# Optimization experiments

Measured on AMD Instinct MI355X. Metric: run time of the kernel, lower is better.

## Reference

```python
import jax, jax.numpy as jnp
import numpy as np

NUM_HEADS = 4
IN_CHANNELS = 128


def setup_inputs() -> dict:
    key = jax.random.key(0)
    k_x, k_wq, k_bq, k_wo, k_bo = jax.random.split(key, 5)
    b, c, h, w = 16, IN_CHANNELS, 32, 32
    x = jax.random.normal(k_x, (b, c, h, w), dtype=jnp.float32)
    # 1x1 convs stored as (out_ch, in_ch) matrices
    w_qkv = jax.random.normal(k_wq, (c * 3 * NUM_HEADS, c), dtype=jnp.float32) * 0.02
    b_qkv = jax.random.normal(k_bq, (c * 3 * NUM_HEADS,), dtype=jnp.float32) * 0.02
    w_out = jax.random.normal(k_wo, (c, c * NUM_HEADS), dtype=jnp.float32) * 0.02
    b_out = jax.random.normal(k_bo, (c,), dtype=jnp.float32) * 0.02
    return {"x": x, "w_qkv": w_qkv, "b_qkv": b_qkv, "w_out": w_out, "b_out": b_out}


def reference(x, w_qkv, b_qkv, w_out, b_out):
    b, c, h, w = x.shape
    nh = NUM_HEADS
    # norm is Identity. 1x1 conv == per-pixel matmul over channels.
    qkv = jnp.einsum('bchw,oc->bohw', x, w_qkv) + b_qkv[None, :, None, None]
    qkv = qkv.reshape(b, nh, 3 * c, h, w)
    q, k, v = qkv[:, :, :c], qkv[:, :, c:2 * c], qkv[:, :, 2 * c:]
    # q, v: (b, nh, c, h, w) -> (b*nh, h*w, c); k -> (b*nh, c, h*w)
    q = q.transpose(0, 1, 3, 4, 2).reshape(b * nh, h * w, c)
    k = k.reshape(b * nh, c, h * w)
    v = v.transpose(0, 1, 3, 4, 2).reshape(b * nh, h * w, c)
    scores = jnp.einsum('bnc,bcm->bnm', q, k) * (c ** -0.5)  # (b*nh, hw, hw)
    attn = jax.nn.softmax(scores, axis=-1)
    out = jnp.einsum('bnm,bmc->bnc', attn, v)  # (b*nh, hw, c)
    out = out.reshape(b, nh, h, w, c).transpose(0, 4, 1, 2, 3).reshape(b, nh * c, h, w)
    out = jnp.einsum('bchw,oc->bohw', out, w_out) + b_out[None, :, None, None]
    return out + x
```

## Files before the change

### kernel.cpp

```cpp
#include <hip/hip_runtime.h>
#include <hip/hip_bf16.h>

typedef float  f32x4_v   __attribute__((ext_vector_type(4)));
typedef float  f32x16_v  __attribute__((ext_vector_type(16)));
typedef __bf16 bf16x8_v  __attribute__((ext_vector_type(8)));
typedef __bf16 bf16x4_v  __attribute__((ext_vector_type(4)));

#define WS_Q  0
#define WS_K  8388608
#define WS_V  16777216
#define WS_O  25165824
#define WS_WP 33554432

__device__ __forceinline__ int aswz(int p) { return ((p & 7) ^ ((p >> 3) & 7)) << 4; }

__device__ __forceinline__ void gload16(const void* g, void* l) {
    __builtin_amdgcn_global_load_lds(
        (const __attribute__((address_space(1))) unsigned int*)g,
        (__attribute__((address_space(3))) unsigned int*)l, 16, 0, 0);
}

__global__ __launch_bounds__(256) void k_permute(const float* __restrict__ w_out,
                                                 __bf16* __restrict__ w_perm) {
    int idx  = blockIdx.x * 256 + threadIdx.x;
    int head = idx >> 14;
    int o    = (idx >> 7) & 127;
    int c    = idx & 127;
    w_perm[idx] = (__bf16)w_out[o * 512 + c * 4 + head];
}

__global__ __launch_bounds__(256) void k_qkv(const float* __restrict__ x,
                                             const float* __restrict__ w_qkv,
                                             const float* __restrict__ b_qkv,
                                             __bf16* __restrict__ q_ws,
                                             __bf16* __restrict__ k_ws,
                                             __bf16* __restrict__ v_ws) {
    __shared__ __bf16 Ash[128 * 128];
    __shared__ __bf16 Bsh[128 * 128];
    const int tid = threadIdx.x;
    const int nt  = blockIdx.x;
    const int mt  = blockIdx.y;
    const int gm0 = mt * 128;
    const int b   = gm0 >> 10;
    const int p0  = gm0 & 1023;
    const int o0  = nt * 128;

    char* Ab = reinterpret_cast<char*>(Ash);
    char* Bb = reinterpret_cast<char*>(Bsh);

    for (int it = 0; it < 16; ++it) {
        int idx = tid + it * 256;
        int c   = idx >> 5;
        int i4  = (idx & 31) << 2;
        float4 v = *reinterpret_cast<const float4*>(x + b * 131072 + c * 1024 + p0 + i4);
        float vv[4] = {v.x, v.y, v.z, v.w};
#pragma unroll
        for (int j = 0; j < 4; ++j) {
            int p = i4 + j;
            int byte = ((p << 8) | (c << 1)) ^ aswz(p);
            *reinterpret_cast<__bf16*>(Ab + byte) = (__bf16)vv[j];
        }
    }
    for (int it = 0; it < 16; ++it) {
        int idx = tid + it * 256;
        int o   = idx >> 5;
        int c4  = (idx & 31) << 2;
        float4 v = *reinterpret_cast<const float4*>(w_qkv + (o0 + o) * 128 + c4);
        bf16x4_v h;
        h[0] = (__bf16)v.x; h[1] = (__bf16)v.y; h[2] = (__bf16)v.z; h[3] = (__bf16)v.w;
        int byte = ((o << 8) | (c4 << 1)) ^ aswz(o);
        *reinterpret_cast<bf16x4_v*>(Bb + byte) = h;
    }
    __syncthreads();

    const int lane = tid & 63;
    const int wv   = tid >> 6;
    const int wm   = (wv >> 1) * 64;
    const int wn   = (wv & 1) * 64;
    const int lr   = lane & 15;
    const int lg   = lane >> 4;

    f32x4_v acc[4][4] = {};
#pragma unroll
    for (int ks = 0; ks < 4; ++ks) {
        bf16x8_v af[4], bfr[4];
#pragma unroll
        for (int mi = 0; mi < 4; ++mi) {
            int row  = wm + mi * 16 + lr;
            int byte = ((row << 8) | (ks << 6) | (lg << 4)) ^ aswz(row);
            af[mi] = *reinterpret_cast<const bf16x8_v*>(Ab + byte);
        }
#pragma unroll
        for (int ni = 0; ni < 4; ++ni) {
            int row  = wn + ni * 16 + lr;
            int byte = ((row << 8) | (ks << 6) | (lg << 4)) ^ aswz(row);
            bfr[ni] = *reinterpret_cast<const bf16x8_v*>(Bb + byte);
        }
#pragma unroll
        for (int mi = 0; mi < 4; ++mi)
#pragma unroll
            for (int ni = 0; ni < 4; ++ni)
                acc[mi][ni] = __builtin_amdgcn_mfma_f32_16x16x32_bf16(af[mi], bfr[ni], acc[mi][ni], 0, 0, 0);
    }

#pragma unroll
    for (int ni = 0; ni < 4; ++ni) {
        int o    = o0 + wn + ni * 16 + lr;
        int head = o / 384;
        int rem  = o - head * 384;
        int type = rem >> 7;
        int ch   = rem & 127;
        float bias = b_qkv[o];
        int bh   = (b << 2) + head;
#pragma unroll
        for (int mi = 0; mi < 4; ++mi) {
            int prow = p0 + wm + mi * 16 + lg * 4;
            f32x4_v a = acc[mi][ni];
            if (type == 0) {
#pragma unroll
                for (int r = 0; r < 4; ++r)
                    q_ws[bh * 131072 + (prow + r) * 128 + ch] =
                        (__bf16)((a[r] + bias) * 0.12751744f);
            } else if (type == 1) {
#pragma unroll
                for (int r = 0; r < 4; ++r)
                    k_ws[bh * 131072 + (prow + r) * 128 + ch] = (__bf16)(a[r] + bias);
            } else {
                bf16x4_v hv;
#pragma unroll
                for (int r = 0; r < 4; ++r) hv[r] = (__bf16)(a[r] + bias);
                *reinterpret_cast<bf16x4_v*>(&v_ws[bh * 131072 + ch * 1024 + prow]) = hv;
            }
        }
    }
}

__device__ __forceinline__ void stage_kv(const __bf16* kg, const __bf16* vg,
                                         __bf16* kl, __bf16* vl, int wv, int lane) {
    const int s16 = lane & 15, r4 = lane >> 4;
    const int s8  = lane & 7,  r8 = lane >> 3;
#pragma unroll
    for (int i = 0; i < 4; ++i) {
        int row = wv * 16 + i * 4 + r4;
        const char* src = (const char*)(kg + row * 128) + ((s16 ^ (row & 7)) << 4);
        char* dst = (char*)kl + (wv * 16 + i * 4) * 256;
        gload16(src, dst);
    }
#pragma unroll
    for (int i = 0; i < 4; ++i) {
        int row = wv * 32 + i * 8 + r8;
        const char* src = (const char*)(vg + row * 1024) + ((s8 ^ (row & 7)) << 4);
        char* dst = (char*)vl + (wv * 32 + i * 8) * 128;
        gload16(src, dst);
    }
}

__global__ __launch_bounds__(256, 2) void k_attn(const __bf16* __restrict__ q_ws,
                                                 const __bf16* __restrict__ k_ws,
                                                 const __bf16* __restrict__ v_ws,
                                                 __bf16* __restrict__ o_ws) {
    __shared__ __bf16 Kbuf[2][64 * 128];
    __shared__ __bf16 Vbuf[2][128 * 64];

    const int tid  = threadIdx.x;
    const int lane = tid & 63;
    const int wv   = tid >> 6;
    const int col  = lane & 31;
    const int hi   = lane >> 5;

    const int id   = blockIdx.x;
    const int bh   = (id & 7) * 8 + (id >> 6);
    const int qt   = (id >> 3) & 7;
    const int base = bh * 131072;
    const int q0w  = qt * 128 + wv * 32;

    bf16x8_v bq[8];
    const __bf16* qp = q_ws + base + (q0w + col) * 128 + hi * 8;
#pragma unroll
    for (int ks = 0; ks < 8; ++ks)
        bq[ks] = *reinterpret_cast<const bf16x8_v*>(qp + ks * 16);

    f32x16_v of[4] = {};
    float m = -1e30f, l = 0.f;

    stage_kv(k_ws + base, v_ws + base, &Kbuf[0][0], &Vbuf[0][0], wv, lane);

    for (int t = 0; t < 16; ++t) {
        const int cur = t & 1;
        if (t < 15) {
            stage_kv(k_ws + base + (t + 1) * 64 * 128, v_ws + base + (t + 1) * 64,
                     &Kbuf[cur ^ 1][0], &Vbuf[cur ^ 1][0], wv, lane);
            asm volatile("s_waitcnt vmcnt(8)" ::: "memory");
        } else {
            asm volatile("s_waitcnt vmcnt(0)" ::: "memory");
        }
        __builtin_amdgcn_s_barrier();
        asm volatile("" ::: "memory");
        __builtin_amdgcn_sched_barrier(0);

        const char* Kl = (const char*)&Kbuf[cur][0];
        const char* Vl = (const char*)&Vbuf[cur][0];

        f32x16_v sa = {}, sb = {};
        __builtin_amdgcn_s_setprio(1);
#pragma unroll
        for (int ks = 0; ks < 8; ++ks) {
            const int sl = 2 * ks + hi;
            bf16x8_v af0 = *reinterpret_cast<const bf16x8_v*>(Kl + col * 256 + ((sl ^ (col & 7)) << 4));
            bf16x8_v af1 = *reinterpret_cast<const bf16x8_v*>(Kl + (32 + col) * 256 + ((sl ^ (col & 7)) << 4));
            sa = __builtin_amdgcn_mfma_f32_32x32x16_bf16(af0, bq[ks], sa, 0, 0, 0);
            sb = __builtin_amdgcn_mfma_f32_32x32x16_bf16(af1, bq[ks], sb, 0, 0, 0);
        }
        __builtin_amdgcn_s_setprio(0);

        float v = sa[0];
#pragma unroll
        for (int r = 1; r < 16; ++r) v = fmaxf(v, sa[r]);
#pragma unroll
        for (int r = 0; r < 16; ++r) v = fmaxf(v, sb[r]);
        float pmax = fmaxf(v, __shfl_xor(v, 32));
        if (!__all(pmax - m <= 8.0f)) {
            float fr = __builtin_amdgcn_exp2f(m - pmax);
            m = pmax;
            l *= fr;
#pragma unroll
            for (int r = 0; r < 16; ++r) {
                float frd = __shfl(fr, (r & 3) + 4 * hi + 8 * (r >> 2));
                of[0][r] *= frd; of[1][r] *= frd; of[2][r] *= frd; of[3][r] *= frd;
            }
        }
        float rs = 0.f;
#pragma unroll
        for (int r = 0; r < 16; ++r) { sa[r] = __builtin_amdgcn_exp2f(sa[r] - m); rs += sa[r]; }
#pragma unroll
        for (int r = 0; r < 16; ++r) { sb[r] = __builtin_amdgcn_exp2f(sb[r] - m); rs += sb[r]; }
        l += rs + __shfl_xor(rs, 32);

        bf16x8_v pa[4];
#pragma unroll
        for (int j = 0; j < 4; ++j) {
            const f32x16_v& sj = (j < 2) ? sa : sb;
            const int ro = 8 * (j & 1);
            unsigned w0, w1, w2, w3;
            asm("v_cvt_pk_bf16_f32 %0, %1, %2" : "=v"(w0) : "v"(sj[ro + 0]), "v"(sj[ro + 1]));
            asm("v_cvt_pk_bf16_f32 %0, %1, %2" : "=v"(w2) : "v"(sj[ro + 4]), "v"(sj[ro + 5]));
            asm("v_cvt_pk_bf16_f32 %0, %1, %2" : "=v"(w1) : "v"(sj[ro + 2]), "v"(sj[ro + 3]));
            asm("v_cvt_pk_bf16_f32 %0, %1, %2" : "=v"(w3) : "v"(sj[ro + 6]), "v"(sj[ro + 7]));
            asm("v_permlane32_swap_b32 %0, %1" : "+v"(w0), "+v"(w2));
            asm("v_permlane32_swap_b32 %0, %1" : "+v"(w1), "+v"(w3));
            union { unsigned u[4]; bf16x8_v h; } cvt;
            cvt.u[0] = w0; cvt.u[1] = w1; cvt.u[2] = w2; cvt.u[3] = w3;
            pa[j] = cvt.h;
        }

        __builtin_amdgcn_s_setprio(1);
#pragma unroll
        for (int n = 0; n < 4; ++n) {
#pragma unroll
            for (int j = 0; j < 4; ++j) {
                int row = 32 * n + col;
                bf16x8_v bv = *reinterpret_cast<const bf16x8_v*>(
                    Vl + row * 128 + (((2 * j + hi) ^ (row & 7)) << 4));
                of[n] = __builtin_amdgcn_mfma_f32_32x32x16_bf16(pa[j], bv, of[n], 0, 0, 0);
            }
        }
        __builtin_amdgcn_s_setprio(0);

        asm volatile("s_waitcnt lgkmcnt(0)" ::: "memory");
        __builtin_amdgcn_sched_barrier(0);
        __builtin_amdgcn_s_barrier();
        asm volatile("" ::: "memory");
        __builtin_amdgcn_sched_barrier(0);
    }

    float linv = 1.0f / l;
#pragma unroll
    for (int r = 0; r < 16; ++r) {
        int qr = (r & 3) + 4 * hi + 8 * (r >> 2);
        float ld = __shfl(linv, qr);
        int qg = q0w + qr;
#pragma unroll
        for (int n = 0; n < 4; ++n)
            o_ws[base + qg * 128 + 32 * n + col] = (__bf16)(of[n][r] * ld);
    }
}

__global__ __launch_bounds__(256) void k_out(const __bf16* __restrict__ o_ws,
                                             const __bf16* __restrict__ w_perm,
                                             const float* __restrict__ b_out,
                                             const float* __restrict__ x,
                                             float* __restrict__ out) {
    __shared__ __bf16 Al[64 * 136];
    __shared__ __bf16 Bl[128 * 136];
    const int tid  = threadIdx.x;
    const int lane = tid & 63, wv = tid >> 6;
    const int lr   = lane & 15, lg = lane >> 4;
    const int mt   = blockIdx.x;
    const int gp0  = mt * 64;
    const int b    = gp0 >> 10;
    const int p0   = gp0 & 1023;

    f32x4_v acc[8] = {};
    for (int kc = 0; kc < 4; ++kc) {
        __syncthreads();
#pragma unroll
        for (int it = 0; it < 4; ++it) {
            int idx = tid + it * 256;
            int rr = idx >> 4, k8 = (idx & 15) * 8;
            *reinterpret_cast<bf16x8_v*>(&Al[rr * 136 + k8]) =
                *reinterpret_cast<const bf16x8_v*>(&o_ws[(b * 4 + kc) * 131072 + (p0 + rr) * 128 + k8]);
        }
#pragma unroll
        for (int it = 0; it < 8; ++it) {
            int idx = tid + it * 256;
            int o = idx >> 4, k8 = (idx & 15) * 8;
            *reinterpret_cast<bf16x8_v*>(&Bl[o * 136 + k8]) =
                *reinterpret_cast<const bf16x8_v*>(&w_perm[kc * 16384 + o * 128 + k8]);
        }
        __syncthreads();
#pragma unroll
        for (int ks = 0; ks < 4; ++ks) {
            bf16x8_v af = *reinterpret_cast<const bf16x8_v*>(&Al[(wv * 16 + lr) * 136 + ks * 32 + lg * 8]);
#pragma unroll
            for (int ni = 0; ni < 8; ++ni) {
                bf16x8_v bf_ = *reinterpret_cast<const bf16x8_v*>(&Bl[(ni * 16 + lr) * 136 + ks * 32 + lg * 8]);
                acc[ni] = __builtin_amdgcn_mfma_f32_16x16x32_bf16(af, bf_, acc[ni], 0, 0, 0);
            }
        }
    }

    int prow = p0 + wv * 16 + lg * 4;
#pragma unroll
    for (int ni = 0; ni < 8; ++ni) {
        int o = ni * 16 + lr;
        float bias = b_out[o];
        float4 xr = *reinterpret_cast<const float4*>(&x[b * 131072 + o * 1024 + prow]);
        float4 res;
        res.x = acc[ni][0] + bias + xr.x;
        res.y = acc[ni][1] + bias + xr.y;
        res.z = acc[ni][2] + bias + xr.z;
        res.w = acc[ni][3] + bias + xr.w;
        *reinterpret_cast<float4*>(&out[b * 131072 + o * 1024 + prow]) = res;
    }
}

extern "C" void kernel_launch(void* const* d_in, const int* in_sizes, int n_in,
                              void* d_out, int out_size, void* d_ws, size_t ws_size,
                              hipStream_t stream) {
    const float* x     = (const float*)d_in[0];
    const float* w_qkv = (const float*)d_in[1];
    const float* b_qkv = (const float*)d_in[2];
    const float* w_out = (const float*)d_in[3];
    const float* b_out = (const float*)d_in[4];
    float* out = (float*)d_out;
    __bf16* ws = (__bf16*)d_ws;

    __bf16* q_ws   = ws + WS_Q;
    __bf16* k_ws   = ws + WS_K;
    __bf16* v_ws   = ws + WS_V;
    __bf16* o_ws   = ws + WS_O;
    __bf16* w_perm = ws + WS_WP;

    k_permute<<<256, 256, 0, stream>>>(w_out, w_perm);
    k_qkv<<<dim3(12, 128), 256, 0, stream>>>(x, w_qkv, b_qkv, q_ws, k_ws, v_ws);
    k_attn<<<512, 256, 0, stream>>>(q_ws, k_ws, v_ws, o_ws);
    k_out<<<256, 256, 0, stream>>>(o_ws, w_perm, b_out, x, out);
}
```

Measured before the change: 92.83 us.

## Fold weight permute into QKV GEMM, reuse x tile, and give attention waves two query tiles

The separate weight-permute kernel is merged into the QKV projection kernel. Each QKV block now loads its x tile into LDS once and loops over six output-channel tiles, where before twelve separate blocks each reloaded it. The attention kernel drops to 128 threads per block, and each wave handles two 32-row query tiles that share the same K/V LDS reads, which doubles reuse of K/V fragments. The trade-off is higher register pressure, fewer waves per CU, and a smaller QKV grid (256 blocks) with less parallelism.

```diff
diff --git a/kernel.cpp b/kernel.cpp
--- a/kernel.cpp
+++ b/kernel.cpp
@@ -20,30 +20,30 @@
         (__attribute__((address_space(3))) unsigned int*)l, 16, 0, 0);
 }
 
-__global__ __launch_bounds__(256) void k_permute(const float* __restrict__ w_out,
-                                                 __bf16* __restrict__ w_perm) {
-    int idx  = blockIdx.x * 256 + threadIdx.x;
-    int head = idx >> 14;
-    int o    = (idx >> 7) & 127;
-    int c    = idx & 127;
-    w_perm[idx] = (__bf16)w_out[o * 512 + c * 4 + head];
-}
-
 __global__ __launch_bounds__(256) void k_qkv(const float* __restrict__ x,
                                              const float* __restrict__ w_qkv,
                                              const float* __restrict__ b_qkv,
                                              __bf16* __restrict__ q_ws,
                                              __bf16* __restrict__ k_ws,
-                                             __bf16* __restrict__ v_ws) {
+                                             __bf16* __restrict__ v_ws,
+                                             const float* __restrict__ w_out,
+                                             __bf16* __restrict__ w_perm) {
     __shared__ __bf16 Ash[128 * 128];
     __shared__ __bf16 Bsh[128 * 128];
-    const int tid = threadIdx.x;
-    const int nt  = blockIdx.x;
-    const int mt  = blockIdx.y;
-    const int gm0 = mt * 128;
-    const int b   = gm0 >> 10;
-    const int p0  = gm0 & 1023;
-    const int o0  = nt * 128;
+    const int tid  = threadIdx.x;
+    const int half = blockIdx.x;
+    const int mt   = blockIdx.y;
+    const int gm0  = mt * 128;
+    const int b    = gm0 >> 10;
+    const int p0   = gm0 & 1023;
+
+    {
+        int gid  = (mt * 2 + half) * 256 + tid;
+        int head = gid >> 14;
+        int o    = (gid >> 7) & 127;
+        int c    = gid & 127;
+        w_perm[gid] = (__bf16)w_out[o * 512 + c * 4 + head];
+    }
 
     char* Ab = reinterpret_cast<char*>(Ash);
     char* Bb = reinterpret_cast<char*>(Bsh);
@@ -61,17 +61,6 @@
             *reinterpret_cast<__bf16*>(Ab + byte) = (__bf16)vv[j];
         }
     }
-    for (int it = 0; it < 16; ++it) {
-        int idx = tid + it * 256;
-        int o   = idx >> 5;
-        int c4  = (idx & 31) << 2;
-        float4 v = *reinterpret_cast<const float4*>(w_qkv + (o0 + o) * 128 + c4);
-        bf16x4_v h;
-        h[0] = (__bf16)v.x; h[1] = (__bf16)v.y; h[2] = (__bf16)v.z; h[3] = (__bf16)v.w;
-        int byte = ((o << 8) | (c4 << 1)) ^ aswz(o);
-        *reinterpret_cast<bf16x4_v*>(Bb + byte) = h;
-    }
-    __syncthreads();
 
     const int lane = tid & 63;
     const int wv   = tid >> 6;
@@ -80,56 +69,72 @@
     const int lr   = lane & 15;
     const int lg   = lane >> 4;
 
-    f32x4_v acc[4][4] = {};
-#pragma unroll
-    for (int ks = 0; ks < 4; ++ks) {
-        bf16x8_v af[4], bfr[4];
-#pragma unroll
-        for (int mi = 0; mi < 4; ++mi) {
-            int row  = wm + mi * 16 + lr;
-            int byte = ((row << 8) | (ks << 6) | (lg << 4)) ^ aswz(row);
-            af[mi] = *reinterpret_cast<const bf16x8_v*>(Ab + byte);
-        }
+    for (int i = 0; i < 6; ++i) {
+        const int o0 = (half * 6 + i) * 128;
+        __syncthreads();
+        for (int it = 0; it < 16; ++it) {
+            int idx = tid + it * 256;
+            int o   = idx >> 5;
+            int c4  = (idx & 31) << 2;
+            float4 v = *reinterpret_cast<const float4*>(w_qkv + (o0 + o) * 128 + c4);
+            bf16x4_v h;
+            h[0] = (__bf16)v.x; h[1] = (__bf16)v.y; h[2] = (__bf16)v.z; h[3] = (__bf16)v.w;
+            int byte = ((o << 8) | (c4 << 1)) ^ aswz(o);
+            *reinterpret_cast<bf16x4_v*>(Bb + byte) = h;
+        }
+        __syncthreads();
+
+        f32x4_v acc[4][4] = {};
+#pragma unroll
+        for (int ks = 0; ks < 4; ++ks) {
+            bf16x8_v af[4], bfr[4];
+#pragma unroll
+            for (int mi = 0; mi < 4; ++mi) {
+                int row  = wm + mi * 16 + lr;
+                int byte = ((row << 8) | (ks << 6) | (lg << 4)) ^ aswz(row);
+                af[mi] = *reinterpret_cast<const bf16x8_v*>(Ab + byte);
+            }
+#pragma unroll
+            for (int ni = 0; ni < 4; ++ni) {
+                int row  = wn + ni * 16 + lr;
+                int byte = ((row << 8) | (ks << 6) | (lg << 4)) ^ aswz(row);
+                bfr[ni] = *reinterpret_cast<const bf16x8_v*>(Bb + byte);
+            }
+#pragma unroll
+            for (int mi = 0; mi < 4; ++mi)
+#pragma unroll
+                for (int ni = 0; ni < 4; ++ni)
+                    acc[mi][ni] = __builtin_amdgcn_mfma_f32_16x16x32_bf16(af[mi], bfr[ni], acc[mi][ni], 0, 0, 0);
+        }
+
 #pragma unroll
         for (int ni = 0; ni < 4; ++ni) {
-            int row  = wn + ni * 16 + lr;
-            int byte = ((row << 8) | (ks << 6) | (lg << 4)) ^ aswz(row);
-            bfr[ni] = *reinterpret_cast<const bf16x8_v*>(Bb + byte);
-        }
-#pragma unroll
-        for (int mi = 0; mi < 4; ++mi)
-#pragma unroll
-            for (int ni = 0; ni < 4; ++ni)
-                acc[mi][ni] = __builtin_amdgcn_mfma_f32_16x16x32_bf16(af[mi], bfr[ni], acc[mi][ni], 0, 0, 0);
-    }
-
-#pragma unroll
-    for (int ni = 0; ni < 4; ++ni) {
-        int o    = o0 + wn + ni * 16 + lr;
-        int head = o / 384;
-        int rem  = o - head * 384;
-        int type = rem >> 7;
-        int ch   = rem & 127;
-        float bias = b_qkv[o];
-        int bh   = (b << 2) + head;
-#pragma unroll
-        for (int mi = 0; mi < 4; ++mi) {
-            int prow = p0 + wm + mi * 16 + lg * 4;
-            f32x4_v a = acc[mi][ni];
-            if (type == 0) {
-#pragma unroll
-                for (int r = 0; r < 4; ++r)
-                    q_ws[bh * 131072 + (prow + r) * 128 + ch] =
-                        (__bf16)((a[r] + bias) * 0.12751744f);
-            } else if (type == 1) {
-#pragma unroll
-                for (int r = 0; r < 4; ++r)
-                    k_ws[bh * 131072 + (prow + r) * 128 + ch] = (__bf16)(a[r] + bias);
-            } else {
-                bf16x4_v hv;
-#pragma unroll
-                for (int r = 0; r < 4; ++r) hv[r] = (__bf16)(a[r] + bias);
-                *reinterpret_cast<bf16x4_v*>(&v_ws[bh * 131072 + ch * 1024 + prow]) = hv;
+            int o    = o0 + wn + ni * 16 + lr;
+            int head = o / 384;
+            int rem  = o - head * 384;
+            int type = rem >> 7;
+            int ch   = rem & 127;
+            float bias = b_qkv[o];
+            int bh   = (b << 2) + head;
+#pragma unroll
+            for (int mi = 0; mi < 4; ++mi) {
+                int prow = p0 + wm + mi * 16 + lg * 4;
+                f32x4_v a = acc[mi][ni];
+                if (type == 0) {
+#pragma unroll
+                    for (int r = 0; r < 4; ++r)
+                        q_ws[bh * 131072 + (prow + r) * 128 + ch] =
+                            (__bf16)((a[r] + bias) * 0.12751744f);
+                } else if (type == 1) {
+#pragma unroll
+                    for (int r = 0; r < 4; ++r)
+                        k_ws[bh * 131072 + (prow + r) * 128 + ch] = (__bf16)(a[r] + bias);
+                } else {
+                    bf16x4_v hv;
+#pragma unroll
+                    for (int r = 0; r < 4; ++r) hv[r] = (__bf16)(a[r] + bias);
+                    *reinterpret_cast<bf16x4_v*>(&v_ws[bh * 131072 + ch * 1024 + prow]) = hv;
+                }
             }
         }
     }
@@ -140,22 +145,65 @@
     const int s16 = lane & 15, r4 = lane >> 4;
     const int s8  = lane & 7,  r8 = lane >> 3;
 #pragma unroll
-    for (int i = 0; i < 4; ++i) {
-        int row = wv * 16 + i * 4 + r4;
+    for (int i = 0; i < 8; ++i) {
+        int row = wv * 32 + i * 4 + r4;
         const char* src = (const char*)(kg + row * 128) + ((s16 ^ (row & 7)) << 4);
-        char* dst = (char*)kl + (wv * 16 + i * 4) * 256;
-        gload16(src, dst);
-    }
-#pragma unroll
-    for (int i = 0; i < 4; ++i) {
-        int row = wv * 32 + i * 8 + r8;
+        gload16(src, (char*)kl + (wv * 32 + i * 4) * 256);
+    }
+#pragma unroll
+    for (int i = 0; i < 8; ++i) {
+        int row = wv * 64 + i * 8 + r8;
         const char* src = (const char*)(vg + row * 1024) + ((s8 ^ (row & 7)) << 4);
-        char* dst = (char*)vl + (wv * 32 + i * 8) * 128;
-        gload16(src, dst);
-    }
-}
-
-__global__ __launch_bounds__(256, 2) void k_attn(const __bf16* __restrict__ q_ws,
+        gload16(src, (char*)vl + (wv * 64 + i * 8) * 128);
+    }
+}
+
+__device__ __forceinline__ void softmax_pack(f32x16_v& s0, f32x16_v& s1,
+                                             float& m, float& l,
+                                             f32x16_v (&of)[4], bf16x8_v (&pa)[4],
+                                             int hi) {
+    float t[16];
+#pragma unroll
+    for (int r = 0; r < 16; ++r) t[r] = fmaxf(s0[r], s1[r]);
+#pragma unroll
+    for (int w = 8; w >= 1; w >>= 1)
+#pragma unroll
+        for (int r = 0; r < w; ++r) t[r] = fmaxf(t[r], t[r + w]);
+    float pmax = fmaxf(t[0], __shfl_xor(t[0], 32));
+    if (!__all(pmax - m <= 8.0f)) {
+        float fr = __builtin_amdgcn_exp2f(m - pmax);
+        m = pmax;
+        l *= fr;
+#pragma unroll
+        for (int r = 0; r < 16; ++r) {
+            float frd = __shfl(fr, (r & 3) + 4 * hi + 8 * (r >> 2));
+            of[0][r] *= frd; of[1][r] *= frd; of[2][r] *= frd; of[3][r] *= frd;
+        }
+    }
+    float rs = 0.f;
+#pragma unroll
+    for (int r = 0; r < 16; ++r) { s0[r] = __builtin_amdgcn_exp2f(s0[r] - m); rs += s0[r]; }
+#pragma unroll
+    for (int r = 0; r < 16; ++r) { s1[r] = __builtin_amdgcn_exp2f(s1[r] - m); rs += s1[r]; }
+    l += rs + __shfl_xor(rs, 32);
+#pragma unroll
+    for (int j = 0; j < 4; ++j) {
+        const f32x16_v& sj = (j < 2) ? s0 : s1;
+        const int ro = 8 * (j & 1);
+        unsigned w0, w1, w2, w3;
+        asm("v_cvt_pk_bf16_f32 %0, %1, %2" : "=v"(w0) : "v"(sj[ro + 0]), "v"(sj[ro + 1]));
+        asm("v_cvt_pk_bf16_f32 %0, %1, %2" : "=v"(w2) : "v"(sj[ro + 4]), "v"(sj[ro + 5]));
+        asm("v_cvt_pk_bf16_f32 %0, %1, %2" : "=v"(w1) : "v"(sj[ro + 2]), "v"(sj[ro + 3]));
+        asm("v_cvt_pk_bf16_f32 %0, %1, %2" : "=v"(w3) : "v"(sj[ro + 6]), "v"(sj[ro + 7]));
+        asm("v_permlane32_swap_b32 %0, %1" : "+v"(w0), "+v"(w2));
+        asm("v_permlane32_swap_b32 %0, %1" : "+v"(w1), "+v"(w3));
+        union { unsigned u[4]; bf16x8_v h; } cvt;
+        cvt.u[0] = w0; cvt.u[1] = w1; cvt.u[2] = w2; cvt.u[3] = w3;
+        pa[j] = cvt.h;
+    }
+}
+
+__global__ __launch_bounds__(128, 1) void k_attn(const __bf16* __restrict__ q_ws,
                                                  const __bf16* __restrict__ k_ws,
                                                  const __bf16* __restrict__ v_ws,
                                                  __bf16* __restrict__ o_ws) {
@@ -172,16 +220,19 @@
     const int bh   = (id & 7) * 8 + (id >> 6);
     const int qt   = (id >> 3) & 7;
     const int base = bh * 131072;
-    const int q0w  = qt * 128 + wv * 32;
-
-    bf16x8_v bq[8];
-    const __bf16* qp = q_ws + base + (q0w + col) * 128 + hi * 8;
-#pragma unroll
-    for (int ks = 0; ks < 8; ++ks)
-        bq[ks] = *reinterpret_cast<const bf16x8_v*>(qp + ks * 16);
-
-    f32x16_v of[4] = {};
-    float m = -1e30f, l = 0.f;
+    const int q0w  = qt * 128 + wv * 64;
+
+    bf16x8_v bqA[8], bqB[8];
+    const __bf16* qpA = q_ws + base + (q0w + col) * 128 + hi * 8;
+    const __bf16* qpB = qpA + 32 * 128;
+#pragma unroll
+    for (int ks = 0; ks < 8; ++ks) {
+        bqA[ks] = *reinterpret_cast<const bf16x8_v*>(qpA + ks * 16);
+        bqB[ks] = *reinterpret_cast<const bf16x8_v*>(qpB + ks * 16);
+    }
+
+    f32x16_v ofA[4] = {}, ofB[4] = {};
+    float mA = -1e30f, lA = 0.f, mB = -1e30f, lB = 0.f;
 
     stage_kv(k_ws + base, v_ws + base, &Kbuf[0][0], &Vbuf[0][0], wv, lane);
 
@@ -190,7 +241,7 @@
         if (t < 15) {
             stage_kv(k_ws + base + (t + 1) * 64 * 128, v_ws + base + (t + 1) * 64,
                      &Kbuf[cur ^ 1][0], &Vbuf[cur ^ 1][0], wv, lane);
-            asm volatile("s_waitcnt vmcnt(8)" ::: "memory");
+            asm volatile("s_waitcnt vmcnt(16)" ::: "memory");
         } else {
             asm volatile("s_waitcnt vmcnt(0)" ::: "memory");
         }
@@ -201,57 +252,23 @@
         const char* Kl = (const char*)&Kbuf[cur][0];
         const char* Vl = (const char*)&Vbuf[cur][0];
 
-        f32x16_v sa = {}, sb = {};
+        f32x16_v sA0 = {}, sA1 = {}, sB0 = {}, sB1 = {};
         __builtin_amdgcn_s_setprio(1);
 #pragma unroll
         for (int ks = 0; ks < 8; ++ks) {
             const int sl = 2 * ks + hi;
             bf16x8_v af0 = *reinterpret_cast<const bf16x8_v*>(Kl + col * 256 + ((sl ^ (col & 7)) << 4));
             bf16x8_v af1 = *reinterpret_cast<const bf16x8_v*>(Kl + (32 + col) * 256 + ((sl ^ (col & 7)) << 4));
-            sa = __builtin_amdgcn_mfma_f32_32x32x16_bf16(af0, bq[ks], sa, 0, 0, 0);
-            sb = __builtin_amdgcn_mfma_f32_32x32x16_bf16(af1, bq[ks], sb, 0, 0, 0);
+            sA0 = __builtin_amdgcn_mfma_f32_32x32x16_bf16(af0, bqA[ks], sA0, 0, 0, 0);
+            sA1 = __builtin_amdgcn_mfma_f32_32x32x16_bf16(af1, bqA[ks], sA1, 0, 0, 0);
+            sB0 = __builtin_amdgcn_mfma_f32_32x32x16_bf16(af0, bqB[ks], sB0, 0, 0, 0);
+            sB1 = __builtin_amdgcn_mfma_f32_32x32x16_bf16(af1, bqB[ks], sB1, 0, 0, 0);
         }
         __builtin_amdgcn_s_setprio(0);
 
-        float v = sa[0];
-#pragma unroll
-        for (int r = 1; r < 16; ++r) v = fmaxf(v, sa[r]);
-#pragma unroll
-        for (int r = 0; r < 16; ++r) v = fmaxf(v, sb[r]);
-        float pmax = fmaxf(v, __shfl_xor(v, 32));
-        if (!__all(pmax - m <= 8.0f)) {
-            float fr = __builtin_amdgcn_exp2f(m - pmax);
-            m = pmax;
-            l *= fr;
-#pragma unroll
-            for (int r = 0; r < 16; ++r) {
-                float frd = __shfl(fr, (r & 3) + 4 * hi + 8 * (r >> 2));
-                of[0][r] *= frd; of[1][r] *= frd; of[2][r] *= frd; of[3][r] *= frd;
-            }
-        }
-        float rs = 0.f;
-#pragma unroll
-        for (int r = 0; r < 16; ++r) { sa[r] = __builtin_amdgcn_exp2f(sa[r] - m); rs += sa[r]; }
-#pragma unroll
-        for (int r = 0; r < 16; ++r) { sb[r] = __builtin_amdgcn_exp2f(sb[r] - m); rs += sb[r]; }
-        l += rs + __shfl_xor(rs, 32);
-
-        bf16x8_v pa[4];
-#pragma unroll
-        for (int j = 0; j < 4; ++j) {
-            const f32x16_v& sj = (j < 2) ? sa : sb;
-            const int ro = 8 * (j & 1);
-            unsigned w0, w1, w2, w3;
-            asm("v_cvt_pk_bf16_f32 %0, %1, %2" : "=v"(w0) : "v"(sj[ro + 0]), "v"(sj[ro + 1]));
-            asm("v_cvt_pk_bf16_f32 %0, %1, %2" : "=v"(w2) : "v"(sj[ro + 4]), "v"(sj[ro + 5]));
-            asm("v_cvt_pk_bf16_f32 %0, %1, %2" : "=v"(w1) : "v"(sj[ro + 2]), "v"(sj[ro + 3]));
-            asm("v_cvt_pk_bf16_f32 %0, %1, %2" : "=v"(w3) : "v"(sj[ro + 6]), "v"(sj[ro + 7]));
-            asm("v_permlane32_swap_b32 %0, %1" : "+v"(w0), "+v"(w2));
-            asm("v_permlane32_swap_b32 %0, %1" : "+v"(w1), "+v"(w3));
-            union { unsigned u[4]; bf16x8_v h; } cvt;
-            cvt.u[0] = w0; cvt.u[1] = w1; cvt.u[2] = w2; cvt.u[3] = w3;
-            pa[j] = cvt.h;
-        }
+        bf16x8_v paA[4], paB[4];
+        softmax_pack(sA0, sA1, mA, lA, ofA, paA, hi);
+        softmax_pack(sB0, sB1, mB, lB, ofB, paB, hi);
 
         __builtin_amdgcn_s_setprio(1);
 #pragma unroll
@@ -261,7 +278,8 @@
                 int row = 32 * n + col;
                 bf16x8_v bv = *reinterpret_cast<const bf16x8_v*>(
                     Vl + row * 128 + (((2 * j + hi) ^ (row & 7)) << 4));
-                of[n] = __builtin_amdgcn_mfma_f32_32x32x16_bf16(pa[j], bv, of[n], 0, 0, 0);
+                ofA[n] = __builtin_amdgcn_mfma_f32_32x32x16_bf16(paA[j], bv, ofA[n], 0, 0, 0);
+                ofB[n] = __builtin_amdgcn_mfma_f32_32x32x16_bf16(paB[j], bv, ofB[n], 0, 0, 0);
             }
         }
         __builtin_amdgcn_s_setprio(0);
@@ -273,15 +291,17 @@
         __builtin_amdgcn_sched_barrier(0);
     }
 
-    float linv = 1.0f / l;
+    float linvA = 1.0f / lA, linvB = 1.0f / lB;
 #pragma unroll
     for (int r = 0; r < 16; ++r) {
         int qr = (r & 3) + 4 * hi + 8 * (r >> 2);
-        float ld = __shfl(linv, qr);
-        int qg = q0w + qr;
-#pragma unroll
-        for (int n = 0; n < 4; ++n)
-            o_ws[base + qg * 128 + 32 * n + col] = (__bf16)(of[n][r] * ld);
+        float ldA = __shfl(linvA, qr);
+        float ldB = __shfl(linvB, qr);
+#pragma unroll
+        for (int n = 0; n < 4; ++n) {
+            o_ws[base + (q0w + qr) * 128 + 32 * n + col]      = (__bf16)(ofA[n][r] * ldA);
+            o_ws[base + (q0w + 32 + qr) * 128 + 32 * n + col] = (__bf16)(ofB[n][r] * ldB);
+        }
     }
 }
 
@@ -361,8 +381,7 @@
     __bf16* o_ws   = ws + WS_O;
     __bf16* w_perm = ws + WS_WP;
 
-    k_permute<<<256, 256, 0, stream>>>(w_out, w_perm);
-    k_qkv<<<dim3(12, 128), 256, 0, stream>>>(x, w_qkv, b_qkv, q_ws, k_ws, v_ws);
-    k_attn<<<512, 256, 0, stream>>>(q_ws, k_ws, v_ws, o_ws);
+    k_qkv<<<dim3(2, 128), 256, 0, stream>>>(x, w_qkv, b_qkv, q_ws, k_ws, v_ws, w_out, w_perm);
+    k_attn<<<512, 128, 0, stream>>>(q_ws, k_ws, v_ws, o_ws);
     k_out<<<256, 256, 0, stream>>>(o_ws, w_perm, b_out, x, out);
 }
```

New measurement: 104.2 us. 1.12x slower.

## Reuse x tile across QKV output tiles, fuse permute, shrink attention KV tile

Applied to the files above, without the earlier changes.

The QKV projection grid shrinks from 12x128 to 2x128 blocks. Each block keeps its converted x tile in shared memory and loops over six weight tiles, and the w_out permute kernel is folded into this kernel, which removes one launch. The attention kernel moves to 128-thread blocks (two waves, 64 queries) with 32-key K/V tiles, twice as many iterations and twice the grid, and declares launch bounds that allow three blocks per unit. The intent is to cut redundant x loads and conversion, drop a launch, and raise attention occupancy. The cost is fewer, serialized QKV blocks and half the MFMA work between each barrier and softmax step in attention.

```diff
diff --git a/kernel.cpp b/kernel.cpp
--- a/kernel.cpp
+++ b/kernel.cpp
@@ -20,30 +20,30 @@
         (__attribute__((address_space(3))) unsigned int*)l, 16, 0, 0);
 }
 
-__global__ __launch_bounds__(256) void k_permute(const float* __restrict__ w_out,
-                                                 __bf16* __restrict__ w_perm) {
-    int idx  = blockIdx.x * 256 + threadIdx.x;
-    int head = idx >> 14;
-    int o    = (idx >> 7) & 127;
-    int c    = idx & 127;
-    w_perm[idx] = (__bf16)w_out[o * 512 + c * 4 + head];
-}
-
 __global__ __launch_bounds__(256) void k_qkv(const float* __restrict__ x,
                                              const float* __restrict__ w_qkv,
                                              const float* __restrict__ b_qkv,
                                              __bf16* __restrict__ q_ws,
                                              __bf16* __restrict__ k_ws,
-                                             __bf16* __restrict__ v_ws) {
+                                             __bf16* __restrict__ v_ws,
+                                             const float* __restrict__ w_out,
+                                             __bf16* __restrict__ w_perm) {
     __shared__ __bf16 Ash[128 * 128];
     __shared__ __bf16 Bsh[128 * 128];
-    const int tid = threadIdx.x;
-    const int nt  = blockIdx.x;
-    const int mt  = blockIdx.y;
-    const int gm0 = mt * 128;
-    const int b   = gm0 >> 10;
-    const int p0  = gm0 & 1023;
-    const int o0  = nt * 128;
+    const int tid  = threadIdx.x;
+    const int half = blockIdx.x;
+    const int mt   = blockIdx.y;
+    const int gm0  = mt * 128;
+    const int b    = gm0 >> 10;
+    const int p0   = gm0 & 1023;
+
+    {
+        int gid  = (mt * 2 + half) * 256 + tid;
+        int head = gid >> 14;
+        int o    = (gid >> 7) & 127;
+        int c    = gid & 127;
+        w_perm[gid] = (__bf16)w_out[o * 512 + c * 4 + head];
+    }
 
     char* Ab = reinterpret_cast<char*>(Ash);
     char* Bb = reinterpret_cast<char*>(Bsh);
@@ -61,17 +61,6 @@
             *reinterpret_cast<__bf16*>(Ab + byte) = (__bf16)vv[j];
         }
     }
-    for (int it = 0; it < 16; ++it) {
-        int idx = tid + it * 256;
-        int o   = idx >> 5;
-        int c4  = (idx & 31) << 2;
-        float4 v = *reinterpret_cast<const float4*>(w_qkv + (o0 + o) * 128 + c4);
-        bf16x4_v h;
-        h[0] = (__bf16)v.x; h[1] = (__bf16)v.y; h[2] = (__bf16)v.z; h[3] = (__bf16)v.w;
-        int byte = ((o << 8) | (c4 << 1)) ^ aswz(o);
-        *reinterpret_cast<bf16x4_v*>(Bb + byte) = h;
-    }
-    __syncthreads();
 
     const int lane = tid & 63;
     const int wv   = tid >> 6;
@@ -80,87 +69,107 @@
     const int lr   = lane & 15;
     const int lg   = lane >> 4;
 
-    f32x4_v acc[4][4] = {};
-#pragma unroll
-    for (int ks = 0; ks < 4; ++ks) {
-        bf16x8_v af[4], bfr[4];
-#pragma unroll
-        for (int mi = 0; mi < 4; ++mi) {
-            int row  = wm + mi * 16 + lr;
-            int byte = ((row << 8) | (ks << 6) | (lg << 4)) ^ aswz(row);
-            af[mi] = *reinterpret_cast<const bf16x8_v*>(Ab + byte);
-        }
+    for (int i = 0; i < 6; ++i) {
+        const int o0 = (half * 6 + i) * 128;
+        __syncthreads();
+        for (int it = 0; it < 16; ++it) {
+            int idx = tid + it * 256;
+            int o   = idx >> 5;
+            int c4  = (idx & 31) << 2;
+            float4 v = *reinterpret_cast<const float4*>(w_qkv + (o0 + o) * 128 + c4);
+            bf16x4_v h;
+            h[0] = (__bf16)v.x; h[1] = (__bf16)v.y; h[2] = (__bf16)v.z; h[3] = (__bf16)v.w;
+            int byte = ((o << 8) | (c4 << 1)) ^ aswz(o);
+            *reinterpret_cast<bf16x4_v*>(Bb + byte) = h;
+        }
+        __syncthreads();
+
+        f32x4_v acc[4][4] = {};
+#pragma unroll
+        for (int ks = 0; ks < 4; ++ks) {
+            bf16x8_v af[4], bfr[4];
+#pragma unroll
+            for (int mi = 0; mi < 4; ++mi) {
+                int row  = wm + mi * 16 + lr;
+                int byte = ((row << 8) | (ks << 6) | (lg << 4)) ^ aswz(row);
+                af[mi] = *reinterpret_cast<const bf16x8_v*>(Ab + byte);
+            }
+#pragma unroll
+            for (int ni = 0; ni < 4; ++ni) {
+                int row  = wn + ni * 16 + lr;
+                int byte = ((row << 8) | (ks << 6) | (lg << 4)) ^ aswz(row);
+                bfr[ni] = *reinterpret_cast<const bf16x8_v*>(Bb + byte);
+            }
+#pragma unroll
+            for (int mi = 0; mi < 4; ++mi)
+#pragma unroll
+                for (int ni = 0; ni < 4; ++ni)
+                    acc[mi][ni] = __builtin_amdgcn_mfma_f32_16x16x32_bf16(af[mi], bfr[ni], acc[mi][ni], 0, 0, 0);
+        }
+
 #pragma unroll
         for (int ni = 0; ni < 4; ++ni) {
-            int row  = wn + ni * 16 + lr;
-            int byte = ((row << 8) | (ks << 6) | (lg << 4)) ^ aswz(row);
-            bfr[ni] = *reinterpret_cast<const bf16x8_v*>(Bb + byte);
-        }
-#pragma unroll
-        for (int mi = 0; mi < 4; ++mi)
-#pragma unroll
-            for (int ni = 0; ni < 4; ++ni)
-                acc[mi][ni] = __builtin_amdgcn_mfma_f32_16x16x32_bf16(af[mi], bfr[ni], acc[mi][ni], 0, 0, 0);
-    }
-
-#pragma unroll
-    for (int ni = 0; ni < 4; ++ni) {
-        int o    = o0 + wn + ni * 16 + lr;
-        int head = o / 384;
-        int rem  = o - head * 384;
-        int type = rem >> 7;
-        int ch   = rem & 127;
-        float bias = b_qkv[o];
-        int bh   = (b << 2) + head;
-#pragma unroll
-        for (int mi = 0; mi < 4; ++mi) {
-            int prow = p0 + wm + mi * 16 + lg * 4;
-            f32x4_v a = acc[mi][ni];
-            if (type == 0) {
-#pragma unroll
-                for (int r = 0; r < 4; ++r)
-                    q_ws[bh * 131072 + (prow + r) * 128 + ch] =
-                        (__bf16)((a[r] + bias) * 0.12751744f);
-            } else if (type == 1) {
-#pragma unroll
-                for (int r = 0; r < 4; ++r)
-                    k_ws[bh * 131072 + (prow + r) * 128 + ch] = (__bf16)(a[r] + bias);
-            } else {
-                bf16x4_v hv;
-#pragma unroll
-                for (int r = 0; r < 4; ++r) hv[r] = (__bf16)(a[r] + bias);
-                *reinterpret_cast<bf16x4_v*>(&v_ws[bh * 131072 + ch * 1024 + prow]) = hv;
-            }
-        }
-    }
-}
-
-__device__ __forceinline__ void stage_kv(const __bf16* kg, const __bf16* vg,
-                                         __bf16* kl, __bf16* vl, int wv, int lane) {
+            int o    = o0 + wn + ni * 16 + lr;
+            int head = o / 384;
+            int rem  = o - head * 384;
+            int type = rem >> 7;
+            int ch   = rem & 127;
+            float bias = b_qkv[o];
+            int bh   = (b << 2) + head;
+#pragma unroll
+            for (int mi = 0; mi < 4; ++mi) {
+                int prow = p0 + wm + mi * 16 + lg * 4;
+                f32x4_v a = acc[mi][ni];
+                if (type == 0) {
+#pragma unroll
+                    for (int r = 0; r < 4; ++r)
+                        q_ws[bh * 131072 + (prow + r) * 128 + ch] =
+                            (__bf16)((a[r] + bias) * 0.12751744f);
+                } else if (type == 1) {
+#pragma unroll
+                    for (int r = 0; r < 4; ++r)
+                        k_ws[bh * 131072 + (prow + r) * 128 + ch] = (__bf16)(a[r] + bias);
+                } else {
+                    bf16x4_v hv;
+#pragma unroll
+                    for (int r = 0; r < 4; ++r) hv[r] = (__bf16)(a[r] + bias);
+                    *reinterpret_cast<bf16x4_v*>(&v_ws[bh * 131072 + ch * 1024 + prow]) = hv;
+                }
+            }
+        }
+    }
+}
+
+__device__ __forceinline__ void stage_kv32(const __bf16* kg, const __bf16* vg,
+                                           __bf16* kl, __bf16* vl, int wv, int lane) {
     const int s16 = lane & 15, r4 = lane >> 4;
-    const int s8  = lane & 7,  r8 = lane >> 3;
+    const int s4  = lane & 3,  r16 = lane >> 2;
+#pragma unroll
+    for (int i = 0; i < 2; ++i) {
+        int row = wv * 16 + i * 8 + r4;
+        int rb  = wv * 16 + i * 8 + ((lane >> 4) & ~0);
+        (void)rb;
+    }
 #pragma unroll
     for (int i = 0; i < 4; ++i) {
         int row = wv * 16 + i * 4 + r4;
         const char* src = (const char*)(kg + row * 128) + ((s16 ^ (row & 7)) << 4);
-        char* dst = (char*)kl + (wv * 16 + i * 4) * 256;
-        gload16(src, dst);
+        gload16(src, (char*)kl + (wv * 16 + i * 4) * 256);
     }
 #pragma unroll
     for (int i = 0; i < 4; ++i) {
-        int row = wv * 32 + i * 8 + r8;
-        const char* src = (const char*)(vg + row * 1024) + ((s8 ^ (row & 7)) << 4);
-        char* dst = (char*)vl + (wv * 32 + i * 8) * 128;
-        gload16(src, dst);
-    }
-}
-
-__global__ __launch_bounds__(256, 2) void k_attn(const __bf16* __restrict__ q_ws,
+        int row = wv * 64 + i * 16 + r16;
+        const char* src = (const char*)(vg + row * 1024) + ((s4 ^ (row & 3)) << 4);
+        gload16(src, (char*)vl + (wv * 64 + i * 16) * 64);
+    }
+}
+
+__global__ __launch_bounds__(128, 3) void k_attn(const __bf16* __restrict__ q_ws,
                                                  const __bf16* __restrict__ k_ws,
                                                  const __bf16* __restrict__ v_ws,
                                                  __bf16* __restrict__ o_ws) {
-    __shared__ __bf16 Kbuf[2][64 * 128];
-    __shared__ __bf16 Vbuf[2][128 * 64];
+    __shared__ __bf16 Kbuf[2][32 * 128];
+    __shared__ __bf16 Vbuf[2][128 * 32];
 
     const int tid  = threadIdx.x;
     const int lane = tid & 63;
@@ -169,10 +178,10 @@
     const int hi   = lane >> 5;
 
     const int id   = blockIdx.x;
-    const int bh   = (id & 7) * 8 + (id >> 6);
-    const int qt   = (id >> 3) & 7;
+    const int bh   = (id & 7) * 8 + (id >> 7);
+    const int qt   = (id >> 3) & 15;
     const int base = bh * 131072;
-    const int q0w  = qt * 128 + wv * 32;
+    const int q0w  = qt * 64 + wv * 32;
 
     bf16x8_v bq[8];
     const __bf16* qp = q_ws + base + (q0w + col) * 128 + hi * 8;
@@ -183,13 +192,13 @@
     f32x16_v of[4] = {};
     float m = -1e30f, l = 0.f;
 
-    stage_kv(k_ws + base, v_ws + base, &Kbuf[0][0], &Vbuf[0][0], wv, lane);
-
-    for (int t = 0; t < 16; ++t) {
+    stage_kv32(k_ws + base, v_ws + base, &Kbuf[0][0], &Vbuf[0][0], wv, lane);
+
+    for (int t = 0; t < 32; ++t) {
         const int cur = t & 1;
-        if (t < 15) {
-            stage_kv(k_ws + base + (t + 1) * 64 * 128, v_ws + base + (t + 1) * 64,
-                     &Kbuf[cur ^ 1][0], &Vbuf[cur ^ 1][0], wv, lane);
+        if (t < 31) {
+            stage_kv32(k_ws + base + (t + 1) * 32 * 128, v_ws + base + (t + 1) * 32,
+                       &Kbuf[cur ^ 1][0], &Vbuf[cur ^ 1][0], wv, lane);
             asm volatile("s_waitcnt vmcnt(8)" ::: "memory");
         } else {
             asm volatile("s_waitcnt vmcnt(0)" ::: "memory");
@@ -201,24 +210,24 @@
         const char* Kl = (const char*)&Kbuf[cur][0];
         const char* Vl = (const char*)&Vbuf[cur][0];
 
-        f32x16_v sa = {}, sb = {};
+        f32x16_v sa = {};
         __builtin_amdgcn_s_setprio(1);
 #pragma unroll
         for (int ks = 0; ks < 8; ++ks) {
             const int sl = 2 * ks + hi;
-            bf16x8_v af0 = *reinterpret_cast<const bf16x8_v*>(Kl + col * 256 + ((sl ^ (col & 7)) << 4));
-            bf16x8_v af1 = *reinterpret_cast<const bf16x8_v*>(Kl + (32 + col) * 256 + ((sl ^ (col & 7)) << 4));
-            sa = __builtin_amdgcn_mfma_f32_32x32x16_bf16(af0, bq[ks], sa, 0, 0, 0);
-            sb = __builtin_amdgcn_mfma_f32_32x32x16_bf16(af1, bq[ks], sb, 0, 0, 0);
+            bf16x8_v af = *reinterpret_cast<const bf16x8_v*>(Kl + col * 256 + ((sl ^ (col & 7)) << 4));
+            sa = __builtin_amdgcn_mfma_f32_32x32x16_bf16(af, bq[ks], sa, 0, 0, 0);
         }
         __builtin_amdgcn_s_setprio(0);
 
-        float v = sa[0];
-#pragma unroll
-        for (int r = 1; r < 16; ++r) v = fmaxf(v, sa[r]);
-#pragma unroll
-        for (int r = 0; r < 16; ++r) v = fmaxf(v, sb[r]);
-        float pmax = fmaxf(v, __shfl_xor(v, 32));
+        float t8[8];
+#pragma unroll
+        for (int r = 0; r < 8; ++r) t8[r] = fmaxf(sa[r], sa[r + 8]);
+#pragma unroll
+        for (int w = 4; w >= 1; w >>= 1)
+#pragma unroll
+            for (int r = 0; r < w; ++r) t8[r] = fmaxf(t8[r], t8[r + w]);
+        float pmax = fmaxf(t8[0], __shfl_xor(t8[0], 32));
         if (!__all(pmax - m <= 8.0f)) {
             float fr = __builtin_amdgcn_exp2f(m - pmax);
             m = pmax;
@@ -232,20 +241,17 @@
         float rs = 0.f;
 #pragma unroll
         for (int r = 0; r < 16; ++r) { sa[r] = __builtin_amdgcn_exp2f(sa[r] - m); rs += sa[r]; }
-#pragma unroll
-        for (int r = 0; r < 16; ++r) { sb[r] = __builtin_amdgcn_exp2f(sb[r] - m); rs += sb[r]; }
         l += rs + __shfl_xor(rs, 32);
 
-        bf16x8_v pa[4];
-#pragma unroll
-        for (int j = 0; j < 4; ++j) {
-            const f32x16_v& sj = (j < 2) ? sa : sb;
-            const int ro = 8 * (j & 1);
+        bf16x8_v pa[2];
+#pragma unroll
+        for (int j = 0; j < 2; ++j) {
+            const int ro = 8 * j;
             unsigned w0, w1, w2, w3;
-            asm("v_cvt_pk_bf16_f32 %0, %1, %2" : "=v"(w0) : "v"(sj[ro + 0]), "v"(sj[ro + 1]));
-            asm("v_cvt_pk_bf16_f32 %0, %1, %2" : "=v"(w2) : "v"(sj[ro + 4]), "v"(sj[ro + 5]));
-            asm("v_cvt_pk_bf16_f32 %0, %1, %2" : "=v"(w1) : "v"(sj[ro + 2]), "v"(sj[ro + 3]));
-            asm("v_cvt_pk_bf16_f32 %0, %1, %2" : "=v"(w3) : "v"(sj[ro + 6]), "v"(sj[ro + 7]));
+            asm("v_cvt_pk_bf16_f32 %0, %1, %2" : "=v"(w0) : "v"(sa[ro + 0]), "v"(sa[ro + 1]));
+            asm("v_cvt_pk_bf16_f32 %0, %1, %2" : "=v"(w2) : "v"(sa[ro + 4]), "v"(sa[ro + 5]));
+            asm("v_cvt_pk_bf16_f32 %0, %1, %2" : "=v"(w1) : "v"(sa[ro + 2]), "v"(sa[ro + 3]));
+            asm("v_cvt_pk_bf16_f32 %0, %1, %2" : "=v"(w3) : "v"(sa[ro + 6]), "v"(sa[ro + 7]));
             asm("v_permlane32_swap_b32 %0, %1" : "+v"(w0), "+v"(w2));
             asm("v_permlane32_swap_b32 %0, %1" : "+v"(w1), "+v"(w3));
             union { unsigned u[4]; bf16x8_v h; } cvt;
@@ -257,10 +263,10 @@
 #pragma unroll
         for (int n = 0; n < 4; ++n) {
 #pragma unroll
-            for (int j = 0; j < 4; ++j) {
+            for (int j = 0; j < 2; ++j) {
                 int row = 32 * n + col;
                 bf16x8_v bv = *reinterpret_cast<const bf16x8_v*>(
-                    Vl + row * 128 + (((2 * j + hi) ^ (row & 7)) << 4));
+                    Vl + row * 64 + (((2 * j + hi) ^ (row & 3)) << 4));
                 of[n] = __builtin_amdgcn_mfma_f32_32x32x16_bf16(pa[j], bv, of[n], 0, 0, 0);
             }
         }
@@ -361,8 +367,7 @@
     __bf16* o_ws   = ws + WS_O;
     __bf16* w_perm = ws + WS_WP;
 
-    k_permute<<<256, 256, 0, stream>>>(w_out, w_perm);
-    k_qkv<<<dim3(12, 128), 256, 0, stream>>>(x, w_qkv, b_qkv, q_ws, k_ws, v_ws);
-    k_attn<<<512, 256, 0, stream>>>(q_ws, k_ws, v_ws, o_ws);
+    k_qkv<<<dim3(2, 128), 256, 0, stream>>>(x, w_qkv, b_qkv, q_ws, k_ws, v_ws, w_out, w_perm);
+    k_attn<<<1024, 128, 0, stream>>>(q_ws, k_ws, v_ws, o_ws);
     k_out<<<256, 256, 0, stream>>>(o_ws, w_perm, b_out, x, out);
 }
```

Result: slower. 100.3 us (+8.0%).
